# Optimization experiments

Measured on AMD Instinct MI355X. Metric: run time of the kernel, lower is better.

Reference implementation:

```python
import jax, jax.numpy as jnp
import numpy as np

B = 64
BAND = 16384
N_OSC = 32
CH = 64
T_IN = 32
N_NOISE_FRAMES = BAND // 4          # 4096
NOISE_STEP = BAND // N_NOISE_FRAMES  # 4 samples per noise frame
NOISE_COEFFS = NOISE_STEP // 2 + 1   # 3 rfft coefficients
N_UP = int(np.log2(N_NOISE_FRAMES) - np.log2(T_IN))  # 7 doubling blocks
LOWEST_FREQ = 20.0 / 11025.0


def _conv1d(x, w, b, pad):
    # x: (B, Cin, T), w: (Cout, Cin, K)
    out = jax.lax.conv_general_dilated(x, w, (1,), [(pad, pad)],
                                       dimension_numbers=('NCH', 'OIH', 'NCH'))
    return out + b[None, :, None]


def _leaky(x):
    return jnp.where(x > 0, x, 0.2 * x)


def _lin_interp(x, size):
    # torch F.interpolate(mode='linear', align_corners=False) along last axis
    n = x.shape[-1]
    coords = (jnp.arange(size, dtype=jnp.float32) + 0.5) * (n / size) - 0.5
    coords = jnp.clip(coords, 0.0, n - 1.0)
    lo = jnp.floor(coords).astype(jnp.int32)
    hi = jnp.minimum(lo + 1, n - 1)
    frac = (coords - lo.astype(jnp.float32)).astype(x.dtype)
    return x[..., lo] * (1.0 - frac) + x[..., hi] * frac


def setup_inputs() -> dict:
    key = jax.random.key(0)
    ks = jax.random.split(key, 16)
    s = 0.1
    return {
        'x': jax.random.normal(ks[0], (B, T_IN, CH), jnp.float32),
        'noise': jax.random.uniform(ks[1], (B, N_NOISE_FRAMES, NOISE_STEP), jnp.float32, -1.0, 1.0),
        'net_w': jax.random.normal(ks[2], (4, CH, CH, 3), jnp.float32) * s,
        'net_b': jax.random.normal(ks[3], (4, CH), jnp.float32) * s,
        'final_w': jax.random.normal(ks[4], (CH, CH, 3), jnp.float32) * s,
        'final_b': jax.random.normal(ks[5], (CH,), jnp.float32) * s,
        'amp_w': jax.random.normal(ks[6], (N_OSC, CH), jnp.float32) * s,
        'amp_b': jax.random.normal(ks[7], (N_OSC,), jnp.float32) * s,
        'freq_w': jax.random.normal(ks[8], (N_OSC, CH), jnp.float32) * s,
        'freq_b': jax.random.normal(ks[9], (N_OSC,), jnp.float32) * s,
        'nz_init_w': jax.random.normal(ks[10], (CH, CH), jnp.float32) * s,
        'nz_init_b': jax.random.normal(ks[11], (CH,), jnp.float32) * s,
        'nz_up_w': jax.random.normal(ks[12], (N_UP, CH, CH, 3), jnp.float32) * s,
        'nz_up_b': jax.random.normal(ks[13], (N_UP, CH), jnp.float32) * s,
        'nz_final_w': jax.random.normal(ks[14], (NOISE_COEFFS, CH), jnp.float32) * s,
        'nz_final_b': jax.random.normal(ks[15], (NOISE_COEFFS,), jnp.float32) * s,
    }


def reference(x, noise, net_w, net_b, final_w, final_b, amp_w, amp_b, freq_w, freq_b,
              nz_init_w, nz_init_b, nz_up_w, nz_up_b, nz_final_w, nz_final_b):
    z = jnp.transpose(x, (0, 2, 1))  # (B, CH, T_IN)
    for i in range(4):
        z = _leaky(_conv1d(z, net_w[i], net_b[i], 1))
    z = _conv1d(z, final_w, final_b, 1)

    # --- OscillatorBank: sigmoid freq (constrained), abs amp, linear upsample,
    # phase accumulation via cumsum, summed sinusoids ---
    amp = jnp.abs(jnp.einsum('bct,oc->bot', z, amp_w) + amp_b[None, :, None])
    freq = jax.nn.sigmoid(jnp.einsum('bct,oc->bot', z, freq_w) + freq_b[None, :, None])
    freq = LOWEST_FREQ + freq * (1.0 - LOWEST_FREQ)
    amp = _lin_interp(amp, BAND)    # (B, N_OSC, BAND)
    freq = _lin_interp(freq, BAND)  # (B, N_OSC, BAND)
    phase = jnp.cumsum(freq * jnp.pi, axis=-1)
    harm = jnp.sum(amp * jnp.sin(phase), axis=1, keepdims=True)  # (B, 1, BAND)

    # 1x1 conv to rfft coeffs, squared, applied per-frame to uniform noise ---
    y = jnp.einsum('bct,oc->bot', z, nz_init_w) + nz_init_b[None, :, None]
    for i in range(N_UP):
        y = jnp.repeat(y, 2, axis=-1)
        y = _leaky(_conv1d(y, nz_up_w[i], nz_up_b[i], 1))
    coeffs = jnp.einsum('bct,oc->bot', y, nz_final_w) + nz_final_b[None, :, None]
    coeffs = coeffs ** 2                      # squared=True, activation=identity
    coeffs = jnp.transpose(coeffs, (0, 2, 1))  # (B, frames, NOISE_COEFFS)
    spec = jnp.fft.rfft(noise, axis=-1, norm='ortho')   # (B, frames, NOISE_COEFFS)
    filt = spec * coeffs.astype(spec.dtype)
    nz = jnp.fft.irfft(filt, n=NOISE_STEP, axis=-1, norm='ortho')  # (B, frames, step)
    nz = nz.reshape(B, 1, BAND)

    return harm + nz
```

## Files before the change

kernel.cpp:

```cpp
#include <hip/hip_runtime.h>
#include <math.h>

#define LOWEST_FREQ_F 0.00181405895691609977f

typedef short bf16x8 __attribute__((ext_vector_type(8)));
typedef float f32x16 __attribute__((ext_vector_type(16)));

__device__ __forceinline__ float lrelu(float x) { return x > 0.f ? x : 0.2f * x; }
__device__ __forceinline__ float sin_rev(float fr) { return __builtin_amdgcn_sinf(fr); }
__device__ __forceinline__ float bf2f(unsigned short u) {
  union { unsigned int i; float f; } x; x.i = ((unsigned int)u) << 16; return x.f;
}
__device__ __forceinline__ unsigned short f2bf(float f) {
  union { float f; unsigned int i; } x; x.f = f;
  unsigned int r = x.i + 0x7FFFu + ((x.i >> 16) & 1u);
  return (unsigned short)(r >> 16);
}
__device__ __forceinline__ unsigned int pack2(float a, float b) {
  return (unsigned int)f2bf(a) | ((unsigned int)f2bf(b) << 16);
}

__global__ __launch_bounds__(256) void prep_kernel(
    const float* __restrict__ net_w, const float* __restrict__ fin_w,
    const float* __restrict__ amp_w, const float* __restrict__ frq_w,
    const float* __restrict__ nzi_w, const float* __restrict__ nzu_w,
    float* __restrict__ wtF4, float* __restrict__ awfwT,
    float* __restrict__ nzT, short* __restrict__ wfold)
{
  __shared__ __align__(16) float wls[12288];
  const int tid = threadIdx.x;
  const int bx  = blockIdx.x;

  if (bx < 7) {
    const float4* src = (const float4*)(nzu_w + bx * 12288);
    #pragma unroll
    for (int i = 0; i < 12; ++i)
      ((float4*)wls)[tid + i*256] = src[tid + i*256];
    __syncthreads();
    short* dst = wfold + bx * 16384;
    for (int i = 0; i < 64; ++i) {
      int q = i*256 + tid;
      int pd = q >> 12, co = (q >> 6) & 63, ci = q & 63;
      const float* wb = wls + co*192 + ci*3;
      float v;
      if      (pd == 0) v = wb[0];
      else if (pd == 1) v = wb[1] + wb[2];
      else if (pd == 2) v = wb[0] + wb[1];
      else              v = wb[2];
      dst[q] = (short)f2bf(v);
    }
  } else if (bx < 12) {
    int l = bx - 7;
    const float* s0 = (l < 4) ? (net_w + l * 12288) : fin_w;
    const float4* src = (const float4*)s0;
    #pragma unroll
    for (int i = 0; i < 12; ++i)
      ((float4*)wls)[tid + i*256] = src[tid + i*256];
    __syncthreads();
    float4* dst = ((float4*)wtF4) + l * 4096;
    for (int i = 0; i < 16; ++i) {
      int q = i*256 + tid;
      int ci = q >> 6, co = q & 63;
      const float* wb = wls + co*192 + ci*3;
      dst[q] = make_float4(wb[0], wb[1], wb[2], 0.f);
    }
  } else {
    #pragma unroll
    for (int i = 0; i < 2; ++i)
      ((float4*)wls)[tid + i*256] = ((const float4*)amp_w)[tid + i*256];
    #pragma unroll
    for (int i = 0; i < 2; ++i)
      ((float4*)(wls + 2048))[tid + i*256] = ((const float4*)frq_w)[tid + i*256];
    #pragma unroll
    for (int i = 0; i < 4; ++i)
      ((float4*)(wls + 4096))[tid + i*256] = ((const float4*)nzi_w)[tid + i*256];
    __syncthreads();
    for (int i = 0; i < 16; ++i) {
      int q = i*256 + tid;
      int c2 = q >> 7, rem = q & 127, o = rem >> 2, k = rem & 3;
      int c = c2*2 + (k >> 1);
      awfwT[q] = (k & 1) ? wls[2048 + o*64 + c] : wls[o*64 + c];
    }
    for (int i = 0; i < 16; ++i) {
      int q = i*256 + tid;
      int c = q >> 6, o = q & 63;
      nzT[q] = wls[4096 + o*64 + c];
    }
  }
}

template<int NT, bool TOGLOBAL>
__device__ __forceinline__ void up_stage2(
    const short* bin, short* bout, unsigned short* gout,
    const short* __restrict__ wf, const float* __restrict__ bias, int tid,
    int roff, int pairbase, int smin, int smax)
{
  const int L  = tid & 63;
  const int w  = tid >> 6;
  const int mt = w & 1;
  const int pg = w >> 1;

  bf16x8 Af[4][4];
  {
    const short* wb = wf + (mt*32 + (L & 31))*64 + ((L >> 5) << 3);
    #pragma unroll
    for (int pd = 0; pd < 4; ++pd)
      #pragma unroll
      for (int ks = 0; ks < 4; ++ks)
        Af[pd][ks] = *(const bf16x8*)(wb + pd*4096 + ks*16);
  }
  f32x16 binit;
  #pragma unroll
  for (int r = 0; r < 16; ++r)
    binit[r] = bias[mt*32 + (r & 3) + 8*(r >> 2) + 4*(L >> 5)];

  for (int n = pg; n < NT; n += 2) {
    int sl = n*32 + (L & 31);
    const short* bp = bin + (sl + roff)*72 + ((L >> 5) << 3);
    f32x16 Ce = binit, Co = binit;
    #pragma unroll
    for (int ks = 0; ks < 4; ++ks) {
      bf16x8 Bm = *(const bf16x8*)(bp + ks*16);
      bf16x8 B0 = *(const bf16x8*)(bp + 72 + ks*16);
      bf16x8 Bp = *(const bf16x8*)(bp + 144 + ks*16);
      Ce = __builtin_amdgcn_mfma_f32_32x32x16_bf16(Af[0][ks], Bm, Ce, 0, 0, 0);
      Ce = __builtin_amdgcn_mfma_f32_32x32x16_bf16(Af[1][ks], B0, Ce, 0, 0, 0);
      Co = __builtin_amdgcn_mfma_f32_32x32x16_bf16(Af[2][ks], B0, Co, 0, 0, 0);
      Co = __builtin_amdgcn_mfma_f32_32x32x16_bf16(Af[3][ks], Bp, Co, 0, 0, 0);
    }
    const int s0 = 2*(sl + pairbase);
    const bool we = (s0 >= smin)     && (s0 < smax);
    const bool wo = (s0 + 1 >= smin) && (s0 + 1 < smax);
    #pragma unroll
    for (int q4 = 0; q4 < 4; ++q4) {
      int co0 = mt*32 + 8*q4 + 4*(L >> 5);
      uint2 ve, vo;
      ve.x = pack2(lrelu(Ce[4*q4+0]), lrelu(Ce[4*q4+1]));
      ve.y = pack2(lrelu(Ce[4*q4+2]), lrelu(Ce[4*q4+3]));
      vo.x = pack2(lrelu(Co[4*q4+0]), lrelu(Co[4*q4+1]));
      vo.y = pack2(lrelu(Co[4*q4+2]), lrelu(Co[4*q4+3]));
      if (TOGLOBAL) {
        if (we) *(uint2*)(gout + (size_t)(2*sl)*64 + co0)     = ve;
        if (wo) *(uint2*)(gout + (size_t)(2*sl + 1)*64 + co0) = vo;
      } else {
        if (we) *(uint2*)&bout[(2*sl)*72 + co0]     = ve;
        if (wo) *(uint2*)&bout[(2*sl + 1)*72 + co0] = vo;
      }
    }
  }
}

__global__ __launch_bounds__(256) void up345(
    const unsigned short* __restrict__ y0g, unsigned short* __restrict__ y6,
    const short* __restrict__ wfold, const float* __restrict__ nzu_b)
{
  __shared__ __align__(16) short arena[521 * 72];
  short* y0b = arena;
  short* y1b = arena + 34*72;
  short* y2b = arena + 69*72;
  short* s3  = arena + 135*72;
  short* s4  = arena + 201*72;
  short* s5  = arena + 329*72;

  const int b   = blockIdx.y;
  const int bx  = blockIdx.x;
  const int tid = threadIdx.x;

  for (int i = tid; i < 4689; i += 256) ((uint4*)arena)[i] = make_uint4(0,0,0,0);
  __syncthreads();

  const unsigned short* inb = y0g + (size_t)b * 32 * 64;
  for (int c = tid; c < 34*8; c += 256) {
    int row = c >> 3, pos = (c & 7) << 3;
    int g = 4*bx - 2 + row;
    if (g >= 0 && g < 32)
      *(bf16x8*)&y0b[row*72 + pos] = *(const bf16x8*)(inb + (size_t)g*64 + pos);
  }
  __syncthreads();

  int lo, hi;
  lo = 8*bx - 2;   hi = 8*bx + 18;
  up_stage2<1,false>(y0b, y1b, nullptr, wfold + 0*16384, nzu_b + 0*64, tid,
                     0, 4*bx - 1, lo < 0 ? 0 : lo, hi > 64 ? 64 : hi);
  __syncthreads();
  lo = 16*bx - 2;  hi = 16*bx + 33;
  up_stage2<1,false>(y1b, y2b, nullptr, wfold + 1*16384, nzu_b + 1*64, tid,
                     0, 8*bx - 1, lo < 0 ? 0 : lo, hi > 128 ? 128 : hi);
  __syncthreads();
  lo = 32*bx - 2;  hi = 32*bx + 64;
  up_stage2<2,false>(y2b, s3, nullptr, wfold + 2*16384, nzu_b + 2*64, tid,
                     0, 16*bx - 1, lo < 0 ? 0 : lo, hi > 256 ? 256 : hi);
  __syncthreads();
  lo = 64*bx - 2;  hi = 64*bx + 126;
  up_stage2<2,false>(s3, s4, nullptr, wfold + 3*16384, nzu_b + 3*64, tid,
                     0, 32*bx - 1, lo < 0 ? 0 : lo, hi > 512 ? 512 : hi);
  __syncthreads();
  lo = 128*bx - 2; hi = 128*bx + 190;
  up_stage2<3,false>(s4, s5, nullptr, wfold + 4*16384, nzu_b + 4*64, tid,
                     0, 64*bx - 1, lo < 0 ? 0 : lo, hi > 1024 ? 1024 : hi);
  __syncthreads();

  unsigned short* outb = y6 + ((size_t)b*2048 + 256*bx) * 64;
  up_stage2<4,true>(s5, nullptr, outb, wfold + 5*16384, nzu_b + 5*64, tid,
                    1, 128*bx, 0, 1 << 30);
}

__device__ __forceinline__ void load_w8(float4* W, const float4* wp, int cc) {
  #pragma unroll
  for (int k = 0; k < 8; ++k) W[k] = wp[(cc*8 + k)*64];
}
__device__ __forceinline__ void load_z8(float* Z, const float* pa, int cc, int t0) {
  #pragma unroll
  for (int k = 0; k < 8; ++k) {
    const float* r = pa + (cc*8 + k)*36 + t0;
    float4 a = *(const float4*)r;
    float2 b2 = *(const float2*)(r + 4);
    Z[k*6+0] = a.x; Z[k*6+1] = a.y; Z[k*6+2] = a.z;
    Z[k*6+3] = a.w; Z[k*6+4] = b2.x; Z[k*6+5] = b2.y;
  }
}
__device__ __forceinline__ void fma8(float* acc, const float4* W, const float* Z) {
  #pragma unroll
  for (int k = 0; k < 8; ++k) {
    #pragma unroll
    for (int j = 0; j < 4; ++j) {
      acc[j] = fmaf(W[k].x, Z[k*6+j],   acc[j]);
      acc[j] = fmaf(W[k].y, Z[k*6+j+1], acc[j]);
      acc[j] = fmaf(W[k].z, Z[k*6+j+2], acc[j]);
    }
  }
}

__global__ __launch_bounds__(512, 2) void z_front(
    const float* __restrict__ x, const float* __restrict__ wtF4,
    const float* __restrict__ net_b, const float* __restrict__ fin_b,
    const float* __restrict__ awfwT, const float* __restrict__ amp_b,
    const float* __restrict__ frq_b,
    const float* __restrict__ nzT, const float* __restrict__ nzi_b,
    unsigned short* __restrict__ y0g, float* __restrict__ amp_o,
    float* __restrict__ frq_o, float* __restrict__ ph_o)
{
  __shared__ __align__(16) char arena[31104];
  float* za = (float*)arena;
  float* zb = (float*)(arena + 9216);
  float* zt = (float*)(arena + 18432);
  float* fl = (float*)(arena + 26880);

  const int b   = blockIdx.x;
  const int tid = threadIdx.x;
  const int co  = tid & 63;
  const int wv  = tid >> 6;

  for (int idx = tid; idx < 2048; idx += 512) {
    int t = idx >> 6, c = idx & 63;
    za[c*36 + t + 1] = x[b*2048 + idx];
  }
  if (tid < 64) {
    za[tid*36] = 0.f; za[tid*36 + 33] = 0.f;
    zb[tid*36] = 0.f; zb[tid*36 + 33] = 0.f;
  }
  __syncthreads();

  float* pa = za;
  float* pb = zb;
  for (int l = 0; l < 5; ++l) {
    {
      const int t0 = wv << 2;
      float bv = (l < 4) ? net_b[l*64 + co] : fin_b[co];
      float acc[4];
      #pragma unroll
      for (int j = 0; j < 4; ++j) acc[j] = bv;

      const float4* wp = ((const float4*)wtF4) + l*4096 + co;
      float4 wA[8], wB[8];
      float  zA[48], zB[48];
      load_w8(wA, wp, 0);
      load_z8(zA, pa, 0, t0);

      #pragma unroll
      for (int cc = 0; cc < 8; ++cc) {
        if (cc & 1) {
          if (cc < 7) { load_w8(wA, wp, cc + 1); load_z8(zA, pa, cc + 1, t0); }
          fma8(acc, wB, zB);
        } else {
          if (cc < 7) { load_w8(wB, wp, cc + 1); load_z8(zB, pa, cc + 1, t0); }
          fma8(acc, wA, zA);
        }
      }

      if (l < 4) {
        #pragma unroll
        for (int j = 0; j < 4; ++j)
          pb[co*36 + t0 + j + 1] = lrelu(acc[j]);
      } else {
        #pragma unroll
        for (int j = 0; j < 4; ++j) {
          int t = t0 + j;
          pb[co*36 + t] = acc[j];
          zt[t*66 + co] = acc[j];
        }
      }
    }
    __syncthreads();
    float* tp = pa; pa = pb; pb = tp;
  }
  const float* zf = pa;

  {
    const int q = wv;
    float bv0 = nzi_b[co];
    float acc[4];
    #pragma unroll
    for (int j = 0; j < 4; ++j) acc[j] = bv0;
    #pragma unroll 8
    for (int c = 0; c < 64; ++c) {
      float4 zv = *(const float4*)(zf + c*36 + (q << 2));
      float wvv = nzT[c*64 + co];
      acc[0] = fmaf(wvv, zv.x, acc[0]);
      acc[1] = fmaf(wvv, zv.y, acc[1]);
      acc[2] = fmaf(wvv, zv.z, acc[2]);
      acc[3] = fmaf(wvv, zv.w, acc[3]);
    }
    unsigned short* yb = y0g + (size_t)b * 2048;
    #pragma unroll
    for (int j = 0; j < 4; ++j)
      yb[((q << 2) + j)*64 + co] = f2bf(acc[j]);
  }

  #pragma unroll
  for (int tt = 0; tt < 2; ++tt) {
    int task = tid + 512*tt;
    int o = task & 31, t = task >> 5;
    float aa = amp_b[o], ff = frq_b[o];
    #pragma unroll 8
    for (int c2 = 0; c2 < 32; ++c2) {
      float4 w4 = ((const float4*)awfwT)[c2*32 + o];
      float2 zv = *(const float2*)(zt + t*66 + c2*2);
      aa = fmaf(w4.x, zv.x, aa); ff = fmaf(w4.y, zv.x, ff);
      aa = fmaf(w4.z, zv.y, aa); ff = fmaf(w4.w, zv.y, ff);
    }
    aa = fabsf(aa);
    float sg = 1.f / (1.f + expf(-ff));
    float fq = LOWEST_FREQ_F + sg * (1.f - LOWEST_FREQ_F);
    amp_o[b*1024 + o*32 + t] = aa;
    frq_o[b*1024 + o*32 + t] = fq;
    fl[o*33 + t] = fq;
  }
  __syncthreads();

  if (wv == 7 && (tid & 63) < 32) {
    const int o = tid & 31;
    double P = 256.0 * (double)fl[o*33];
    double hd = P * 0.5;
    ph_o[b*1024 + o*32] = (float)(hd - floor(hd));
    for (int i = 1; i < 32; ++i) {
      P += 256.0 * ((double)fl[o*33 + i - 1] + (double)fl[o*33 + i]);
      hd = P * 0.5;
      ph_o[b*1024 + o*32 + i] = (float)(hd - floor(hd));
    }
  }
}

__global__ __launch_bounds__(256) void final_fused(
    const unsigned short* __restrict__ in,
    const short* __restrict__ wf, const float* __restrict__ bias,
    const float* __restrict__ nzf_w, const float* __restrict__ nzf_b,
    const float* __restrict__ noise,
    const float* __restrict__ amp, const float* __restrict__ frq,
    const float* __restrict__ ph, float* __restrict__ out)
{
  constexpr int STILE = 128, Tin = 2048, ROWS = STILE + 2, G = STILE / 64;
  __shared__ __align__(16) short lB[ROWS * 72];
  __shared__ float al[1024], fqv[1024], pl[1024];
  __shared__ float wl4[256];
  __shared__ float cf[2][3][256];

  const int b   = blockIdx.y;
  const int s0  = blockIdx.x * STILE;
  const int tid = threadIdx.x;
  const int L   = tid & 63;
  const int w   = tid >> 6;
  const int mt  = w & 1;
  const int ng  = w >> 1;

  for (int i = tid; i < 1024; i += 256) {
    al[i]  = amp[b*1024 + i];
    fqv[i] = frq[b*1024 + i];
    pl[i]  = ph[b*1024 + i];
  }
  if (tid < 64) {
    wl4[tid*4 + 0] = nzf_w[tid];
    wl4[tid*4 + 1] = nzf_w[64 + tid];
    wl4[tid*4 + 2] = nzf_w[128 + tid];
    wl4[tid*4 + 3] = 0.f;
  }

  bf16x8 Af[4][4];
  {
    const short* wb = wf + (mt*32 + (L & 31))*64 + ((L >> 5) << 3);
    #pragma unroll
    for (int pd = 0; pd < 4; ++pd)
      #pragma unroll
      for (int ks = 0; ks < 4; ++ks)
        Af[pd][ks] = *(const bf16x8*)(wb + pd*4096 + ks*16);
  }

  const unsigned short* inb = in + (size_t)b * Tin * 64;
  for (int c = tid; c < ROWS*8; c += 256) {
    int row = c >> 3, pos = (c & 7) << 3;
    int g = s0 - 1 + row;
    bf16x8 v = {0,0,0,0,0,0,0,0};
    if (g >= 0 && g < Tin) v = *(const bf16x8*)(inb + (size_t)g*64 + pos);
    *(bf16x8*)&lB[row*72 + pos] = v;
  }

  f32x16 binit;
  #pragma unroll
  for (int r = 0; r < 16; ++r)
    binit[r] = bias[mt*32 + (r & 3) + 8*(r >> 2) + 4*(L >> 5)];

  __syncthreads();

  #pragma unroll
  for (int nt = 0; nt < G; ++nt) {
    int s_loc = ng*(32*G) + nt*32 + (L & 31);
    const short* bp = lB + s_loc*72 + ((L >> 5) << 3);
    f32x16 Ce = binit, Co = binit;
    #pragma unroll
    for (int ks = 0; ks < 4; ++ks) {
      bf16x8 Bm = *(const bf16x8*)(bp + ks*16);
      bf16x8 B0 = *(const bf16x8*)(bp + 72 + ks*16);
      bf16x8 Bp = *(const bf16x8*)(bp + 144 + ks*16);
      Ce = __builtin_amdgcn_mfma_f32_32x32x16_bf16(Af[0][ks], Bm, Ce, 0, 0, 0);
      Ce = __builtin_amdgcn_mfma_f32_32x32x16_bf16(Af[1][ks], B0, Ce, 0, 0, 0);
      Co = __builtin_amdgcn_mfma_f32_32x32x16_bf16(Af[2][ks], B0, Co, 0, 0, 0);
      Co = __builtin_amdgcn_mfma_f32_32x32x16_bf16(Af[3][ks], Bp, Co, 0, 0, 0);
    }
    float c0e = 0.f, c1e = 0.f, c2e = 0.f;
    float c0o = 0.f, c1o = 0.f, c2o = 0.f;
    #pragma unroll
    for (int r = 0; r < 16; ++r) {
      int ch = mt*32 + 8*(r >> 2) + 4*(L >> 5) + (r & 3);
      float4 w4 = *(const float4*)&wl4[ch*4];
      float ye = lrelu(Ce[r]);
      float yo = lrelu(Co[r]);
      c0e = fmaf(w4.x, ye, c0e); c1e = fmaf(w4.y, ye, c1e); c2e = fmaf(w4.z, ye, c2e);
      c0o = fmaf(w4.x, yo, c0o); c1o = fmaf(w4.y, yo, c1o); c2o = fmaf(w4.z, yo, c2o);
    }
    c0e += __shfl_xor(c0e, 32, 64); c1e += __shfl_xor(c1e, 32, 64);
    c2e += __shfl_xor(c2e, 32, 64); c0o += __shfl_xor(c0o, 32, 64);
    c1o += __shfl_xor(c1o, 32, 64); c2o += __shfl_xor(c2o, 32, 64);
    if (L < 32) {
      int fe = 2*s_loc, fo = fe + 1;
      cf[mt][0][fe] = c0e; cf[mt][1][fe] = c1e; cf[mt][2][fe] = c2e;
      cf[mt][0][fo] = c0o; cf[mt][1][fo] = c1o; cf[mt][2][fo] = c2o;
    }
  }
  __syncthreads();

  {
    float c0 = nzf_b[0] + cf[0][0][tid] + cf[1][0][tid];
    float c1 = nzf_b[1] + cf[0][1][tid] + cf[1][1][tid];
    float c2 = nzf_b[2] + cf[0][2][tid] + cf[1][2][tid];
    c0 *= c0; c1 *= c1; c2 *= c2;

    const int fb = 2*s0 + tid;
    const float4 n = *(const float4*)(noise + ((size_t)b*4096 + fb)*4);
    float F0  = c0 * (n.x + n.y + n.z + n.w) * 0.5f;
    float F1r = c1 * (n.x - n.z) * 0.5f;
    float F1i = -(c1 * (n.y - n.w) * 0.5f);
    float F2  = c2 * (n.x - n.y + n.z - n.w) * 0.5f;
    float r0 = 0.5f * (F0 + 2.f*F1r + F2);
    float r1 = 0.5f * (F0 - 2.f*F1i - F2);
    float r2 = 0.5f * (F0 - 2.f*F1r + F2);
    float r3 = 0.5f * (F0 + 2.f*F1i - F2);

    const int t0 = fb * 4;
    float s0a = 0.f, s1a = 0.f, s2a = 0.f, s3a = 0.f;
    if (t0 < 256) {
      const float tp = (float)(t0 + 1) * 0.5f;
      #pragma unroll 4
      for (int o = 0; o < 32; ++o) {
        float f0 = fqv[o*32], am = al[o*32];
        float hf = 0.5f * f0;
        float v0 = tp * f0, v1 = v0 + hf, v2 = v1 + hf, v3 = v2 + hf;
        s0a += am * sin_rev(v0 - floorf(v0));
        s1a += am * sin_rev(v1 - floorf(v1));
        s2a += am * sin_rev(v2 - floorf(v2));
        s3a += am * sin_rev(v3 - floorf(v3));
      }
    } else if (t0 >= 16128) {
      const float tp = (float)(t0 - 16127) * 0.5f;
      #pragma unroll 4
      for (int o = 0; o < 32; ++o) {
        float f0 = fqv[o*32 + 31], am = al[o*32 + 31], p = pl[o*32 + 31];
        float hf = 0.5f * f0;
        float v0 = p + tp * f0, v1 = v0 + hf, v2 = v1 + hf, v3 = v2 + hf;
        s0a += am * sin_rev(v0 - floorf(v0));
        s1a += am * sin_rev(v1 - floorf(v1));
        s2a += am * sin_rev(v2 - floorf(v2));
        s3a += am * sin_rev(v3 - floorf(v3));
      }
    } else {
      const int i  = (t0 - 256) >> 9;
      const int m0 = (t0 - 256) & 511;
      float mm[4], fa[4], mq[4];
      #pragma unroll
      for (int js = 0; js < 4; ++js) {
        float mmv = (float)(m0 + 1 + js);
        mm[js] = mmv;
        fa[js] = ((float)(m0 + js) + 0.5f) * (1.f/512.f);
        mq[js] = mmv * mmv * (1.f/1024.f);
      }
      #pragma unroll 4
      for (int o = 0; o < 32; ++o) {
        float f0 = fqv[o*32 + i], f1 = fqv[o*32 + i + 1];
        float a0 = al[o*32 + i],  a1 = al[o*32 + i + 1];
        float p  = pl[o*32 + i];
        float df = f1 - f0, da = a1 - a0;
        #pragma unroll
        for (int js = 0; js < 4; ++js) {
          float av   = fmaf(da, fa[js], a0);
          float part = fmaf(df, mq[js], mm[js] * f0);
          float v    = fmaf(part, 0.5f, p);
          float fr   = v - floorf(v);
          float sv   = av * sin_rev(fr);
          if      (js == 0) s0a += sv;
          else if (js == 1) s1a += sv;
          else if (js == 2) s2a += sv;
          else              s3a += sv;
        }
      }
    }
    float4 res = make_float4(s0a + r0, s1a + r1, s2a + r2, s3a + r3);
    *(float4*)(out + ((size_t)b*4096 + fb)*4) = res;
  }
}

extern "C" void kernel_launch(void* const* d_in, const int* in_sizes, int n_in,
                              void* d_out, int out_size, void* d_ws, size_t ws_size,
                              hipStream_t stream) {
  (void)in_sizes; (void)n_in; (void)out_size; (void)ws_size;
  const float* x     = (const float*)d_in[0];
  const float* noise = (const float*)d_in[1];
  const float* net_w = (const float*)d_in[2];
  const float* net_b = (const float*)d_in[3];
  const float* fin_w = (const float*)d_in[4];
  const float* fin_b = (const float*)d_in[5];
  const float* amp_w = (const float*)d_in[6];
  const float* amp_b = (const float*)d_in[7];
  const float* frq_w = (const float*)d_in[8];
  const float* frq_b = (const float*)d_in[9];
  const float* nzi_w = (const float*)d_in[10];
  const float* nzi_b = (const float*)d_in[11];
  const float* nzu_w = (const float*)d_in[12];
  const float* nzu_b = (const float*)d_in[13];
  const float* nzf_w = (const float*)d_in[14];
  const float* nzf_b = (const float*)d_in[15];
  float* out = (float*)d_out;

  short* y0    = (short*)d_ws;
  short* y6    = y0 + (size_t)64*32*64;
  short* wfold = y6 + (size_t)64*2048*64;
  float* wtF4  = (float*)(wfold + 7*16384);
  float* awfwT = wtF4 + 81920;
  float* nzT   = awfwT + 4096;
  float* ampv  = nzT + 4096;
  float* frqv  = ampv + 65536;
  float* phv   = frqv + 65536;

  prep_kernel<<<dim3(13), dim3(256), 0, stream>>>(
      net_w, fin_w, amp_w, frq_w, nzi_w, nzu_w, wtF4, awfwT, nzT, wfold);

  z_front<<<dim3(64), dim3(512), 0, stream>>>(
      x, wtF4, net_b, fin_b, awfwT, amp_b, frq_b, nzT, nzi_b,
      (unsigned short*)y0, ampv, frqv, phv);

  up345<<<dim3(8, 64), dim3(256), 0, stream>>>(
      (unsigned short*)y0, (unsigned short*)y6, wfold, nzu_b);

  final_fused<<<dim3(16, 64), dim3(256), 0, stream>>>(
      (unsigned short*)y6, wfold + 6*16384, nzu_b + 6*64,
      nzf_w, nzf_b, noise, ampv, frqv, phv, out);
}
```

Measured before the change: 189.8 us.

## Fuse last two upsample stages and coeff projection into up345

The final upsample stage and the 1x1 projection to squared noise coefficients move into the up345 kernel, computed from LDS. Before, a bf16 activation tensor of 2048x64 per batch went to global memory and the final kernel reloaded it. Now up345 writes only three float coefficients per frame, and the oscillator/noise kernel just reads them. In exchange, the up345 blocks do more serial work at lower parallelism (512 blocks), and the final kernel loses its MFMA work, so overlap between convolution and sine work inside one kernel is lost.

```diff
diff --git a/kernel.cpp b/kernel.cpp
--- a/kernel.cpp
+++ b/kernel.cpp
@@ -89,9 +89,9 @@
   }
 }
 
-template<int NT, bool TOGLOBAL>
+template<int NT>
 __device__ __forceinline__ void up_stage2(
-    const short* bin, short* bout, unsigned short* gout,
+    const short* bin, short* bout,
     const short* __restrict__ wf, const float* __restrict__ bias, int tid,
     int roff, int pairbase, int smin, int smax)
 {
@@ -139,33 +139,101 @@
       ve.y = pack2(lrelu(Ce[4*q4+2]), lrelu(Ce[4*q4+3]));
       vo.x = pack2(lrelu(Co[4*q4+0]), lrelu(Co[4*q4+1]));
       vo.y = pack2(lrelu(Co[4*q4+2]), lrelu(Co[4*q4+3]));
-      if (TOGLOBAL) {
-        if (we) *(uint2*)(gout + (size_t)(2*sl)*64 + co0)     = ve;
-        if (wo) *(uint2*)(gout + (size_t)(2*sl + 1)*64 + co0) = vo;
-      } else {
-        if (we) *(uint2*)&bout[(2*sl)*72 + co0]     = ve;
-        if (wo) *(uint2*)&bout[(2*sl + 1)*72 + co0] = vo;
-      }
+      if (we) *(uint2*)&bout[(2*sl)*72 + co0]     = ve;
+      if (wo) *(uint2*)&bout[(2*sl + 1)*72 + co0] = vo;
+    }
+  }
+}
+
+__device__ __forceinline__ void up_stage_coef(
+    const short* bin, const short* __restrict__ wf,
+    const float* __restrict__ bias, const float* __restrict__ wl4,
+    float* __restrict__ cf, int tid)
+{
+  const int L  = tid & 63;
+  const int w  = tid >> 6;
+  const int mt = w & 1;
+  const int pg = w >> 1;
+
+  bf16x8 Af[4][4];
+  {
+    const short* wb = wf + (mt*32 + (L & 31))*64 + ((L >> 5) << 3);
+    #pragma unroll
+    for (int pd = 0; pd < 4; ++pd)
+      #pragma unroll
+      for (int ks = 0; ks < 4; ++ks)
+        Af[pd][ks] = *(const bf16x8*)(wb + pd*4096 + ks*16);
+  }
+  f32x16 binit;
+  #pragma unroll
+  for (int r = 0; r < 16; ++r)
+    binit[r] = bias[mt*32 + (r & 3) + 8*(r >> 2) + 4*(L >> 5)];
+
+  for (int n = pg; n < 8; n += 2) {
+    int sl = n*32 + (L & 31);
+    const short* bp = bin + (sl + 1)*72 + ((L >> 5) << 3);
+    f32x16 Ce = binit, Co = binit;
+    #pragma unroll
+    for (int ks = 0; ks < 4; ++ks) {
+      bf16x8 Bm = *(const bf16x8*)(bp + ks*16);
+      bf16x8 B0 = *(const bf16x8*)(bp + 72 + ks*16);
+      bf16x8 Bp = *(const bf16x8*)(bp + 144 + ks*16);
+      Ce = __builtin_amdgcn_mfma_f32_32x32x16_bf16(Af[0][ks], Bm, Ce, 0, 0, 0);
+      Ce = __builtin_amdgcn_mfma_f32_32x32x16_bf16(Af[1][ks], B0, Ce, 0, 0, 0);
+      Co = __builtin_amdgcn_mfma_f32_32x32x16_bf16(Af[2][ks], B0, Co, 0, 0, 0);
+      Co = __builtin_amdgcn_mfma_f32_32x32x16_bf16(Af[3][ks], Bp, Co, 0, 0, 0);
+    }
+    float c0e = 0.f, c1e = 0.f, c2e = 0.f;
+    float c0o = 0.f, c1o = 0.f, c2o = 0.f;
+    #pragma unroll
+    for (int r = 0; r < 16; ++r) {
+      int ch = mt*32 + 8*(r >> 2) + 4*(L >> 5) + (r & 3);
+      float4 w4 = *(const float4*)&wl4[ch*4];
+      float ye = lrelu(Ce[r]);
+      float yo = lrelu(Co[r]);
+      c0e = fmaf(w4.x, ye, c0e); c1e = fmaf(w4.y, ye, c1e); c2e = fmaf(w4.z, ye, c2e);
+      c0o = fmaf(w4.x, yo, c0o); c1o = fmaf(w4.y, yo, c1o); c2o = fmaf(w4.z, yo, c2o);
+    }
+    c0e += __shfl_xor(c0e, 32, 64); c1e += __shfl_xor(c1e, 32, 64);
+    c2e += __shfl_xor(c2e, 32, 64); c0o += __shfl_xor(c0o, 32, 64);
+    c1o += __shfl_xor(c1o, 32, 64); c2o += __shfl_xor(c2o, 32, 64);
+    if (L < 32) {
+      int fe = 2*sl, fo = fe + 1;
+      cf[mt*1536 + fe]        = c0e; cf[mt*1536 + 512 + fe]  = c1e;
+      cf[mt*1536 + 1024 + fe] = c2e;
+      cf[mt*1536 + fo]        = c0o; cf[mt*1536 + 512 + fo]  = c1o;
+      cf[mt*1536 + 1024 + fo] = c2o;
     }
   }
 }
 
 __global__ __launch_bounds__(256) void up345(
-    const unsigned short* __restrict__ y0g, unsigned short* __restrict__ y6,
-    const short* __restrict__ wfold, const float* __restrict__ nzu_b)
+    const unsigned short* __restrict__ y0g,
+    const short* __restrict__ wfold, const float* __restrict__ nzu_b,
+    const float* __restrict__ nzf_w, const float* __restrict__ nzf_b,
+    float* __restrict__ csq)
 {
   __shared__ __align__(16) short arena[521 * 72];
+  __shared__ float wl4[256];
   short* y0b = arena;
   short* y1b = arena + 34*72;
   short* y2b = arena + 69*72;
   short* s3  = arena + 135*72;
   short* s4  = arena + 201*72;
   short* s5  = arena + 329*72;
+  short* s6  = arena;
+  float* cf  = (float*)(arena + 329*72);
 
   const int b   = blockIdx.y;
   const int bx  = blockIdx.x;
   const int tid = threadIdx.x;
 
+  if (tid < 64) {
+    wl4[tid*4 + 0] = nzf_w[tid];
+    wl4[tid*4 + 1] = nzf_w[64 + tid];
+    wl4[tid*4 + 2] = nzf_w[128 + tid];
+    wl4[tid*4 + 3] = 0.f;
+  }
   for (int i = tid; i < 4689; i += 256) ((uint4*)arena)[i] = make_uint4(0,0,0,0);
   __syncthreads();
 
@@ -180,29 +248,49 @@
 
   int lo, hi;
   lo = 8*bx - 2;   hi = 8*bx + 18;
-  up_stage2<1,false>(y0b, y1b, nullptr, wfold + 0*16384, nzu_b + 0*64, tid,
-                     0, 4*bx - 1, lo < 0 ? 0 : lo, hi > 64 ? 64 : hi);
+  up_stage2<1>(y0b, y1b, wfold + 0*16384, nzu_b + 0*64, tid,
+               0, 4*bx - 1, lo < 0 ? 0 : lo, hi > 64 ? 64 : hi);
   __syncthreads();
   lo = 16*bx - 2;  hi = 16*bx + 33;
-  up_stage2<1,false>(y1b, y2b, nullptr, wfold + 1*16384, nzu_b + 1*64, tid,
-                     0, 8*bx - 1, lo < 0 ? 0 : lo, hi > 128 ? 128 : hi);
+  up_stage2<1>(y1b, y2b, wfold + 1*16384, nzu_b + 1*64, tid,
+               0, 8*bx - 1, lo < 0 ? 0 : lo, hi > 128 ? 128 : hi);
   __syncthreads();
   lo = 32*bx - 2;  hi = 32*bx + 64;
-  up_stage2<2,false>(y2b, s3, nullptr, wfold + 2*16384, nzu_b + 2*64, tid,
-                     0, 16*bx - 1, lo < 0 ? 0 : lo, hi > 256 ? 256 : hi);
+  up_stage2<2>(y2b, s3, wfold + 2*16384, nzu_b + 2*64, tid,
+               0, 16*bx - 1, lo < 0 ? 0 : lo, hi > 256 ? 256 : hi);
   __syncthreads();
   lo = 64*bx - 2;  hi = 64*bx + 126;
-  up_stage2<2,false>(s3, s4, nullptr, wfold + 3*16384, nzu_b + 3*64, tid,
-                     0, 32*bx - 1, lo < 0 ? 0 : lo, hi > 512 ? 512 : hi);
+  up_stage2<2>(s3, s4, wfold + 3*16384, nzu_b + 3*64, tid,
+               0, 32*bx - 1, lo < 0 ? 0 : lo, hi > 512 ? 512 : hi);
   __syncthreads();
   lo = 128*bx - 2; hi = 128*bx + 190;
-  up_stage2<3,false>(s4, s5, nullptr, wfold + 4*16384, nzu_b + 4*64, tid,
-                     0, 64*bx - 1, lo < 0 ? 0 : lo, hi > 1024 ? 1024 : hi);
-  __syncthreads();
-
-  unsigned short* outb = y6 + ((size_t)b*2048 + 256*bx) * 64;
-  up_stage2<4,true>(s5, nullptr, outb, wfold + 5*16384, nzu_b + 5*64, tid,
-                    1, 128*bx, 0, 1 << 30);
+  up_stage2<3>(s4, s5, wfold + 4*16384, nzu_b + 4*64, tid,
+               0, 64*bx - 1, lo < 0 ? 0 : lo, hi > 1024 ? 1024 : hi);
+  __syncthreads();
+
+  for (int i = tid; i < 2340; i += 256) ((uint4*)arena)[i] = make_uint4(0,0,0,0);
+  __syncthreads();
+
+  hi = 256*bx + 258;
+  up_stage2<5>(s5, s6, wfold + 5*16384, nzu_b + 5*64, tid,
+               0, 128*bx - 1, 0, hi > 2048 ? 2048 : hi);
+  __syncthreads();
+
+  up_stage_coef(s6, wfold + 6*16384, nzu_b + 6*64, wl4, cf, tid);
+  __syncthreads();
+
+  {
+    float b0 = nzf_b[0], b1 = nzf_b[1], b2 = nzf_b[2];
+    for (int i = tid; i < 512; i += 256) {
+      float c0 = b0 + cf[i]        + cf[1536 + i];
+      float c1 = b1 + cf[512 + i]  + cf[1536 + 512 + i];
+      float c2 = b2 + cf[1024 + i] + cf[1536 + 1024 + i];
+      size_t base = (size_t)b*4096 + 512*bx + i;
+      csq[base]            = c0 * c0;
+      csq[262144 + base]   = c1 * c1;
+      csq[524288 + base]   = c2 * c2;
+    }
+  }
 }
 
 __device__ __forceinline__ void load_w8(float4* W, const float4* wp, int cc) {
@@ -361,180 +449,99 @@
   }
 }
 
-__global__ __launch_bounds__(256) void final_fused(
-    const unsigned short* __restrict__ in,
-    const short* __restrict__ wf, const float* __restrict__ bias,
-    const float* __restrict__ nzf_w, const float* __restrict__ nzf_b,
+__global__ __launch_bounds__(256) void osc_noise(
+    const float* __restrict__ csq,
     const float* __restrict__ noise,
     const float* __restrict__ amp, const float* __restrict__ frq,
     const float* __restrict__ ph, float* __restrict__ out)
 {
-  constexpr int STILE = 128, Tin = 2048, ROWS = STILE + 2, G = STILE / 64;
-  __shared__ __align__(16) short lB[ROWS * 72];
   __shared__ float al[1024], fqv[1024], pl[1024];
-  __shared__ float wl4[256];
-  __shared__ float cf[2][3][256];
 
   const int b   = blockIdx.y;
-  const int s0  = blockIdx.x * STILE;
   const int tid = threadIdx.x;
-  const int L   = tid & 63;
-  const int w   = tid >> 6;
-  const int mt  = w & 1;
-  const int ng  = w >> 1;
+  const int fb  = blockIdx.x * 256 + tid;
 
   for (int i = tid; i < 1024; i += 256) {
     al[i]  = amp[b*1024 + i];
     fqv[i] = frq[b*1024 + i];
     pl[i]  = ph[b*1024 + i];
   }
-  if (tid < 64) {
-    wl4[tid*4 + 0] = nzf_w[tid];
-    wl4[tid*4 + 1] = nzf_w[64 + tid];
-    wl4[tid*4 + 2] = nzf_w[128 + tid];
-    wl4[tid*4 + 3] = 0.f;
-  }
-
-  bf16x8 Af[4][4];
-  {
-    const short* wb = wf + (mt*32 + (L & 31))*64 + ((L >> 5) << 3);
-    #pragma unroll
-    for (int pd = 0; pd < 4; ++pd)
-      #pragma unroll
-      for (int ks = 0; ks < 4; ++ks)
-        Af[pd][ks] = *(const bf16x8*)(wb + pd*4096 + ks*16);
-  }
-
-  const unsigned short* inb = in + (size_t)b * Tin * 64;
-  for (int c = tid; c < ROWS*8; c += 256) {
-    int row = c >> 3, pos = (c & 7) << 3;
-    int g = s0 - 1 + row;
-    bf16x8 v = {0,0,0,0,0,0,0,0};
-    if (g >= 0 && g < Tin) v = *(const bf16x8*)(inb + (size_t)g*64 + pos);
-    *(bf16x8*)&lB[row*72 + pos] = v;
-  }
-
-  f32x16 binit;
-  #pragma unroll
-  for (int r = 0; r < 16; ++r)
-    binit[r] = bias[mt*32 + (r & 3) + 8*(r >> 2) + 4*(L >> 5)];
-
-  __syncthreads();
-
-  #pragma unroll
-  for (int nt = 0; nt < G; ++nt) {
-    int s_loc = ng*(32*G) + nt*32 + (L & 31);
-    const short* bp = lB + s_loc*72 + ((L >> 5) << 3);
-    f32x16 Ce = binit, Co = binit;
-    #pragma unroll
-    for (int ks = 0; ks < 4; ++ks) {
-      bf16x8 Bm = *(const bf16x8*)(bp + ks*16);
-      bf16x8 B0 = *(const bf16x8*)(bp + 72 + ks*16);
-      bf16x8 Bp = *(const bf16x8*)(bp + 144 + ks*16);
-      Ce = __builtin_amdgcn_mfma_f32_32x32x16_bf16(Af[0][ks], Bm, Ce, 0, 0, 0);
-      Ce = __builtin_amdgcn_mfma_f32_32x32x16_bf16(Af[1][ks], B0, Ce, 0, 0, 0);
-      Co = __builtin_amdgcn_mfma_f32_32x32x16_bf16(Af[2][ks], B0, Co, 0, 0, 0);
-      Co = __builtin_amdgcn_mfma_f32_32x32x16_bf16(Af[3][ks], Bp, Co, 0, 0, 0);
-    }
-    float c0e = 0.f, c1e = 0.f, c2e = 0.f;
-    float c0o = 0.f, c1o = 0.f, c2o = 0.f;
-    #pragma unroll
-    for (int r = 0; r < 16; ++r) {
-      int ch = mt*32 + 8*(r >> 2) + 4*(L >> 5) + (r & 3);
-      float4 w4 = *(const float4*)&wl4[ch*4];
-      float ye = lrelu(Ce[r]);
-      float yo = lrelu(Co[r]);
-      c0e = fmaf(w4.x, ye, c0e); c1e = fmaf(w4.y, ye, c1e); c2e = fmaf(w4.z, ye, c2e);
-      c0o = fmaf(w4.x, yo, c0o); c1o = fmaf(w4.y, yo, c1o); c2o = fmaf(w4.z, yo, c2o);
-    }
-    c0e += __shfl_xor(c0e, 32, 64); c1e += __shfl_xor(c1e, 32, 64);
-    c2e += __shfl_xor(c2e, 32, 64); c0o += __shfl_xor(c0o, 32, 64);
-    c1o += __shfl_xor(c1o, 32, 64); c2o += __shfl_xor(c2o, 32, 64);
-    if (L < 32) {
-      int fe = 2*s_loc, fo = fe + 1;
-      cf[mt][0][fe] = c0e; cf[mt][1][fe] = c1e; cf[mt][2][fe] = c2e;
-      cf[mt][0][fo] = c0o; cf[mt][1][fo] = c1o; cf[mt][2][fo] = c2o;
-    }
-  }
-  __syncthreads();
-
-  {
-    float c0 = nzf_b[0] + cf[0][0][tid] + cf[1][0][tid];
-    float c1 = nzf_b[1] + cf[0][1][tid] + cf[1][1][tid];
-    float c2 = nzf_b[2] + cf[0][2][tid] + cf[1][2][tid];
-    c0 *= c0; c1 *= c1; c2 *= c2;
-
-    const int fb = 2*s0 + tid;
-    const float4 n = *(const float4*)(noise + ((size_t)b*4096 + fb)*4);
-    float F0  = c0 * (n.x + n.y + n.z + n.w) * 0.5f;
-    float F1r = c1 * (n.x - n.z) * 0.5f;
-    float F1i = -(c1 * (n.y - n.w) * 0.5f);
-    float F2  = c2 * (n.x - n.y + n.z - n.w) * 0.5f;
-    float r0 = 0.5f * (F0 + 2.f*F1r + F2);
-    float r1 = 0.5f * (F0 - 2.f*F1i - F2);
-    float r2 = 0.5f * (F0 - 2.f*F1r + F2);
-    float r3 = 0.5f * (F0 + 2.f*F1i - F2);
-
-    const int t0 = fb * 4;
-    float s0a = 0.f, s1a = 0.f, s2a = 0.f, s3a = 0.f;
-    if (t0 < 256) {
-      const float tp = (float)(t0 + 1) * 0.5f;
-      #pragma unroll 4
-      for (int o = 0; o < 32; ++o) {
-        float f0 = fqv[o*32], am = al[o*32];
-        float hf = 0.5f * f0;
-        float v0 = tp * f0, v1 = v0 + hf, v2 = v1 + hf, v3 = v2 + hf;
-        s0a += am * sin_rev(v0 - floorf(v0));
-        s1a += am * sin_rev(v1 - floorf(v1));
-        s2a += am * sin_rev(v2 - floorf(v2));
-        s3a += am * sin_rev(v3 - floorf(v3));
-      }
-    } else if (t0 >= 16128) {
-      const float tp = (float)(t0 - 16127) * 0.5f;
-      #pragma unroll 4
-      for (int o = 0; o < 32; ++o) {
-        float f0 = fqv[o*32 + 31], am = al[o*32 + 31], p = pl[o*32 + 31];
-        float hf = 0.5f * f0;
-        float v0 = p + tp * f0, v1 = v0 + hf, v2 = v1 + hf, v3 = v2 + hf;
-        s0a += am * sin_rev(v0 - floorf(v0));
-        s1a += am * sin_rev(v1 - floorf(v1));
-        s2a += am * sin_rev(v2 - floorf(v2));
-        s3a += am * sin_rev(v3 - floorf(v3));
-      }
-    } else {
-      const int i  = (t0 - 256) >> 9;
-      const int m0 = (t0 - 256) & 511;
-      float mm[4], fa[4], mq[4];
+  __syncthreads();
+
+  const size_t base = (size_t)b*4096 + fb;
+  float c0 = csq[base];
+  float c1 = csq[262144 + base];
+  float c2 = csq[524288 + base];
+
+  const float4 n = *(const float4*)(noise + base*4);
+  float F0  = c0 * (n.x + n.y + n.z + n.w) * 0.5f;
+  float F1r = c1 * (n.x - n.z) * 0.5f;
+  float F1i = -(c1 * (n.y - n.w) * 0.5f);
+  float F2  = c2 * (n.x - n.y + n.z - n.w) * 0.5f;
+  float r0 = 0.5f * (F0 + 2.f*F1r + F2);
+  float r1 = 0.5f * (F0 - 2.f*F1i - F2);
+  float r2 = 0.5f * (F0 - 2.f*F1r + F2);
+  float r3 = 0.5f * (F0 + 2.f*F1i - F2);
+
+  const int t0 = fb * 4;
+  float s0a = 0.f, s1a = 0.f, s2a = 0.f, s3a = 0.f;
+  if (t0 < 256) {
+    const float tp = (float)(t0 + 1) * 0.5f;
+    #pragma unroll 4
+    for (int o = 0; o < 32; ++o) {
+      float f0 = fqv[o*32], am = al[o*32];
+      float hf = 0.5f * f0;
+      float v0 = tp * f0, v1 = v0 + hf, v2 = v1 + hf, v3 = v2 + hf;
+      s0a += am * sin_rev(v0 - floorf(v0));
+      s1a += am * sin_rev(v1 - floorf(v1));
+      s2a += am * sin_rev(v2 - floorf(v2));
+      s3a += am * sin_rev(v3 - floorf(v3));
+    }
+  } else if (t0 >= 16128) {
+    const float tp = (float)(t0 - 16127) * 0.5f;
+    #pragma unroll 4
+    for (int o = 0; o < 32; ++o) {
+      float f0 = fqv[o*32 + 31], am = al[o*32 + 31], p = pl[o*32 + 31];
+      float hf = 0.5f * f0;
+      float v0 = p + tp * f0, v1 = v0 + hf, v2 = v1 + hf, v3 = v2 + hf;
+      s0a += am * sin_rev(v0 - floorf(v0));
+      s1a += am * sin_rev(v1 - floorf(v1));
+      s2a += am * sin_rev(v2 - floorf(v2));
+      s3a += am * sin_rev(v3 - floorf(v3));
+    }
+  } else {
+    const int i  = (t0 - 256) >> 9;
+    const int m0 = (t0 - 256) & 511;
+    float mm[4], fa[4], mq[4];
+    #pragma unroll
+    for (int js = 0; js < 4; ++js) {
+      float mmv = (float)(m0 + 1 + js);
+      mm[js] = mmv;
+      fa[js] = ((float)(m0 + js) + 0.5f) * (1.f/512.f);
+      mq[js] = mmv * mmv * (1.f/1024.f);
+    }
+    #pragma unroll 4
+    for (int o = 0; o < 32; ++o) {
+      float f0 = fqv[o*32 + i], f1 = fqv[o*32 + i + 1];
+      float a0 = al[o*32 + i],  a1 = al[o*32 + i + 1];
+      float p  = pl[o*32 + i];
+      float df = f1 - f0, da = a1 - a0;
       #pragma unroll
       for (int js = 0; js < 4; ++js) {
-        float mmv = (float)(m0 + 1 + js);
-        mm[js] = mmv;
-        fa[js] = ((float)(m0 + js) + 0.5f) * (1.f/512.f);
-        mq[js] = mmv * mmv * (1.f/1024.f);
+        float av   = fmaf(da, fa[js], a0);
+        float part = fmaf(df, mq[js], mm[js] * f0);
+        float v    = fmaf(part, 0.5f, p);
+        float fr   = v - floorf(v);
+        float sv   = av * sin_rev(fr);
+        if      (js == 0) s0a += sv;
+        else if (js == 1) s1a += sv;
+        else if (js == 2) s2a += sv;
+        else              s3a += sv;
       }
-      #pragma unroll 4
-      for (int o = 0; o < 32; ++o) {
-        float f0 = fqv[o*32 + i], f1 = fqv[o*32 + i + 1];
-        float a0 = al[o*32 + i],  a1 = al[o*32 + i + 1];
-        float p  = pl[o*32 + i];
-        float df = f1 - f0, da = a1 - a0;
-        #pragma unroll
-        for (int js = 0; js < 4; ++js) {
-          float av   = fmaf(da, fa[js], a0);
-          float part = fmaf(df, mq[js], mm[js] * f0);
-          float v    = fmaf(part, 0.5f, p);
-          float fr   = v - floorf(v);
-          float sv   = av * sin_rev(fr);
-          if      (js == 0) s0a += sv;
-          else if (js == 1) s1a += sv;
-          else if (js == 2) s2a += sv;
-          else              s3a += sv;
-        }
-      }
-    }
-    float4 res = make_float4(s0a + r0, s1a + r1, s2a + r2, s3a + r3);
-    *(float4*)(out + ((size_t)b*4096 + fb)*4) = res;
-  }
+    }
+  }
+  float4 res = make_float4(s0a + r0, s1a + r1, s2a + r2, s3a + r3);
+  *(float4*)(out + base*4) = res;
 }
 
 extern "C" void kernel_launch(void* const* d_in, const int* in_sizes, int n_in,
@@ -560,14 +567,14 @@
   float* out = (float*)d_out;
 
   short* y0    = (short*)d_ws;
-  short* y6    = y0 + (size_t)64*32*64;
-  short* wfold = y6 + (size_t)64*2048*64;
+  short* wfold = y0 + (size_t)64*32*64;
   float* wtF4  = (float*)(wfold + 7*16384);
   float* awfwT = wtF4 + 81920;
   float* nzT   = awfwT + 4096;
   float* ampv  = nzT + 4096;
   float* frqv  = ampv + 65536;
   float* phv   = frqv + 65536;
+  float* csq   = phv + 65536;
 
   prep_kernel<<<dim3(13), dim3(256), 0, stream>>>(
       net_w, fin_w, amp_w, frq_w, nzi_w, nzu_w, wtF4, awfwT, nzT, wfold);
@@ -577,9 +584,8 @@
       (unsigned short*)y0, ampv, frqv, phv);
 
   up345<<<dim3(8, 64), dim3(256), 0, stream>>>(
-      (unsigned short*)y0, (unsigned short*)y6, wfold, nzu_b);
-
-  final_fused<<<dim3(16, 64), dim3(256), 0, stream>>>(
-      (unsigned short*)y6, wfold + 6*16384, nzu_b + 6*64,
-      nzf_w, nzf_b, noise, ampv, frqv, phv, out);
-}
+      (unsigned short*)y0, wfold, nzu_b, nzf_w, nzf_b, csq);
+
+  osc_noise<<<dim3(16, 64), dim3(256), 0, stream>>>(
+      csq, noise, ampv, frqv, phv, out);
+}
```

Result: faster. 177.6 us (-6.5%).
